# Kernel tuning notes

Hardware: AMD Instinct MI355X
Metric: run time of the kernel (lower is better)

The kernel has to match this reference:

```python
import jax, jax.numpy as jnp
import numpy as np

# Each of the 16 differentiable binary logic ops op_k(a,b) is a polynomial
# c0 + ca*a + cb*b + cab*(a*b). Rows follow the standard difflogic op table
# (op 3 = 'a' pass-through, matching the residual init in the source).
_OP2POLY = np.array([
    [0, 0, 0, 0],    # 0: False
    [0, 0, 0, 1],    # 1: a AND b
    [0, 1, 0, -1],   # 2: a AND NOT b
    [0, 1, 0, 0],    # 3: a
    [0, 0, 1, -1],   # 4: NOT a AND b
    [0, 0, 1, 0],    # 5: b
    [0, 1, 1, -2],   # 6: XOR
    [0, 1, 1, -1],   # 7: OR
    [1, -1, -1, 1],  # 8: NOR
    [1, -1, -1, 2],  # 9: XNOR
    [1, 0, -1, 0],   # 10: NOT b
    [1, 0, -1, 1],   # 11: a OR NOT b
    [1, -1, 0, 0],   # 12: NOT a
    [1, -1, 0, 1],   # 13: NOT a OR b
    [1, 0, 0, -1],   # 14: NAND
    [1, 0, 0, 0],    # 15: True
], dtype=np.float32)

KERNEL_SIZE, STRIDE, PADDING, GROUPS, TREE_DEPTH, TAU = 3, 1, 1, 1, 4, 1.0


def setup_inputs() -> dict:
    key = jax.random.key(0)
    k0, k1, k2, k3, k4 = jax.random.split(key, 5)
    B, Cin, H, W = 16, 64, 64, 64
    OC, N = 128, 2 ** TREE_DEPTH
    x = jax.random.uniform(k0, (B, Cin, H, W), dtype=jnp.float32)
    weights = jax.random.normal(k1, (OC, N - 1, 16), dtype=jnp.float32)
    ci = jax.random.randint(k2, (OC, N), 0, Cin // GROUPS, dtype=jnp.int32)
    px = jax.random.randint(k3, (OC, N), 0, KERNEL_SIZE, dtype=jnp.int32)
    py = jax.random.randint(k4, (OC, N), 0, KERNEL_SIZE, dtype=jnp.int32)
    return {"x": x, "weights": weights, "input_channel_indices": ci,
            "input_pos_x_indices": px, "input_pos_y_indices": py}


def _forward(x, weights, ci, px, py):
    B, Cin, H, W = x.shape
    OC = weights.shape[0]
    N = 2 ** TREE_DEPTH
    # Training-mode weights with straight-through estimator:
    # value = one_hot(argmax), gradient flows through softmax.
    w_soft = jax.nn.softmax(weights / TAU, axis=-1).astype(x.dtype)
    w_hard = jax.nn.one_hot(jnp.argmax(weights, axis=-1), 16, dtype=x.dtype)
    w = w_soft + jax.lax.stop_gradient(w_hard - w_soft)
    # [OC, num_gates, 4] polynomial coefficients over (1, a, b, ab)
    coeffs = jnp.einsum('ogk,kc->ogc', w, jnp.asarray(_OP2POLY, x.dtype))

    xp = jnp.pad(x, ((0, 0), (0, 0), (PADDING, PADDING), (PADDING, PADDING)))
    oh = (H + 2 * PADDING - KERNEL_SIZE) // STRIDE + 1
    ow = (W + 2 * PADDING - KERNEL_SIZE) // STRIDE + 1

    icpg = Cin // GROUPS
    group_of_oc = jnp.arange(OC, dtype=jnp.int32) // (OC // GROUPS)
    chan = group_of_oc[:, None] * icpg + ci                       # [OC, N]
    rows = (jnp.arange(oh, dtype=jnp.int32) * STRIDE)[None, None, :] + py[:, :, None]  # [OC,N,oh]
    cols = (jnp.arange(ow, dtype=jnp.int32) * STRIDE)[None, None, :] + px[:, :, None]  # [OC,N,ow]
    # Irregular per-output gather: [B, OC, N, oh, ow]
    vals = xp[:, chan[:, :, None, None], rows[:, :, :, None], cols[:, :, None, :]]

    # Binary tree of logic gates, level by level (gates stored leaf-level first).
    gate_off = 0
    for _ in range(TREE_DEPTH):
        n = vals.shape[2] // 2
        a, b = vals[:, :, 0::2], vals[:, :, 1::2]
        cc = coeffs[:, gate_off:gate_off + n]                     # [OC, n, 4]
        c0, ca, cb, cab = (cc[None, :, :, i, None, None] for i in range(4))
        vals = c0 + ca * a + cb * b + cab * (a * b)
        gate_off += n
    y = vals[:, :, 0]                                             # [B, OC, oh, ow]

    # 2x2 OR-pool (soft OR = 1 - prod(1 - v)), floor division of spatial dims.
    ph, pw = oh // 2, ow // 2
    y = y[:, :, :ph * 2, :pw * 2].reshape(B, OC, ph, 2, pw, 2)
    return 1.0 - jnp.prod(1.0 - y, axis=(3, 5))


def reference(x, weights, input_channel_indices, input_pos_x_indices, input_pos_y_indices):
    return _forward(x, weights, input_channel_indices, input_pos_x_indices, input_pos_y_indices)
```

## Files before the change

kernel.cpp:

```cpp
#include <hip/hip_runtime.h>

#define BATCH 16
#define CIN   64
#define H_    64
#define W_    64
#define IMG   (H_ * W_)
#define OCH   128
#define NLEAF 16
#define NGATE 15
#define PH    32
#define PW    32

#define XS_F   0
#define LEAF_F 24576
#define OPS_F  26624
#define ZF     27136
#define SMEM_F 27520

__device__ __constant__ __align__(16) float OP2POLY[16][4] = {
    {0, 0, 0, 0}, {0, 0, 0, 1}, {0, 1, 0, -1}, {0, 1, 0, 0},
    {0, 0, 1, -1}, {0, 0, 1, 0}, {0, 1, 1, -2}, {0, 1, 1, -1},
    {1, -1, -1, 1}, {1, -1, -1, 2}, {1, 0, -1, 0}, {1, 0, -1, 1},
    {1, -1, 0, 0}, {1, -1, 0, 1}, {1, 0, 0, -1}, {1, 0, 0, 0}};

static __device__ __forceinline__ int rfl_i(int v) {
    return __builtin_amdgcn_readfirstlane(v);
}

__global__ __launch_bounds__(1024) void logic_tree_lds(
    const float* __restrict__ x,
    const float* __restrict__ weights,
    const int* __restrict__ ci,
    const int* __restrict__ px,
    const int* __restrict__ py,
    float* __restrict__ out)
{
    __shared__ float smem[SMEM_F];
    int* smem_i = (int*)smem;
    unsigned char* smem_b = (unsigned char*)smem;

    const int blk   = blockIdx.x;
    const int b     = blk >> 4;
    const int strip = blk & 15;
    const int r0    = strip << 2;
    const int tid   = threadIdx.x;

    const float4* xb4 = reinterpret_cast<const float4*>(x + (size_t)b * (CIN * IMG));
#pragma unroll
    for (int i = 0; i < 6; ++i) {
        int fidx = tid + i * 1024;
        int ch   = fidx / 96;
        int rem  = fidx - ch * 96;
        int row  = rem >> 4;
        int c4   = rem & 15;
        int gr   = r0 - 1 + row;
        float4 val = make_float4(0.f, 0.f, 0.f, 0.f);
        if ((unsigned)gr < (unsigned)H_)
            val = xb4[((ch << 6) | gr) * 16 + c4];
        *reinterpret_cast<float4*>(&smem[ch * 384 + row * 64 + c4 * 4]) = val;
    }

    if (tid < 384) smem[ZF + tid] = 0.0f;

    for (int t = tid; t < OCH * NGATE; t += 1024) {
        const float* wp = weights + t * 16;
        int best = 0;
        float bv = wp[0];
#pragma unroll
        for (int k = 1; k < 16; ++k) {
            float v = wp[k];
            if (v > bv) { bv = v; best = k; }
        }
        int oc = t / 15, g = t - oc * 15;
        smem_b[OPS_F * 4 + oc * 16 + g] = (unsigned char)best;
        if (g == 14) smem_b[OPS_F * 4 + oc * 16 + 15] = 0;
    }

    for (int t = tid; t < OCH * NLEAF; t += 1024)
        smem_i[LEAF_F + t] = (ci[t] << 4) | (py[t] << 2) | px[t];

    __syncthreads();

    const int wave = tid >> 6;
    const int lane = tid & 63;

#pragma unroll 1
    for (int q = 0; q < 8; ++q) {
        const int oc = wave * 8 + q;

        const uint4 opsv =
            *reinterpret_cast<const uint4*>(&smem[OPS_F + oc * 4]);
        const unsigned ou[4] = {
            (unsigned)rfl_i((int)opsv.x), (unsigned)rfl_i((int)opsv.y),
            (unsigned)rfl_i((int)opsv.z), (unsigned)rfl_i((int)opsv.w)};
        float C[NGATE * 4];
#pragma unroll
        for (int g = 0; g < NGATE; ++g) {
            int op = (ou[g >> 2] >> ((g & 3) * 8)) & 255;
            const float4 cf = reinterpret_cast<const float4*>(OP2POLY)[op];
            C[4 * g + 0] = cf.x;
            C[4 * g + 1] = cf.y;
            C[4 * g + 2] = cf.z;
            C[4 * g + 3] = cf.w;
        }

        int base[NLEAF];
#pragma unroll
        for (int n = 0; n < NLEAF; ++n) {
            int pk = rfl_i(smem_i[LEAF_F + oc * 16 + n]);
            int ch = pk >> 4;
            int dy = ((pk >> 2) & 3) - 1;
            int dx = (pk & 3) - 1;
            int c  = lane + dx;
            int ccl = min(max(c, 0), W_ - 1);
            int bin = ch * 384 + (1 + dy) * 64 + ccl;
            int bz  = ZF + (1 + dy) * 64 + lane;
            base[n] = ((unsigned)c < (unsigned)W_) ? bin : bz;
        }

        const size_t obase =
            (((size_t)b * OCH + oc) * PH + (r0 >> 1)) * PW + (lane >> 1);

        float pprev = 0.0f;
#pragma unroll
        for (int r = 0; r < 4; ++r) {
            float v[NLEAF];
#pragma unroll
            for (int n = 0; n < NLEAF; ++n)
                v[n] = smem[base[n] + r * 64];

            int go = 0;
#pragma unroll
            for (int lev = 8; lev >= 1; lev >>= 1) {
#pragma unroll
                for (int t = 0; t < lev; ++t) {
                    float a  = v[2 * t];
                    float bb = v[2 * t + 1];
                    v[t] = C[(go + t) * 4] + C[(go + t) * 4 + 1] * a +
                           C[(go + t) * 4 + 2] * bb +
                           C[(go + t) * 4 + 3] * (a * bb);
                }
                go += lev;
            }

            float qv = 1.0f - v[0];
            if (r & 1) {
                float p  = pprev * qv;
                float pp = p * __shfl_xor(p, 1, 64);
                if (!(lane & 1))
                    out[obase + (size_t)(r >> 1) * PW] = 1.0f - pp;
            } else {
                pprev = qv;
            }
        }
    }
}

extern "C" void kernel_launch(void* const* d_in, const int* in_sizes, int n_in,
                              void* d_out, int out_size, void* d_ws, size_t ws_size,
                              hipStream_t stream) {
    const float* x       = (const float*)d_in[0];
    const float* weights = (const float*)d_in[1];
    const int*   ci      = (const int*)d_in[2];
    const int*   px      = (const int*)d_in[3];
    const int*   py      = (const int*)d_in[4];
    float* out = (float*)d_out;
    (void)d_ws; (void)ws_size;

    logic_tree_lds<<<BATCH * 16, 1024, 0, stream>>>(x, weights, ci, px, py, out);
}
```

Baseline: 101.0 us.

## Split weight argmax and leaf descriptors into a prep kernel, use packed float2 tree evaluation

Moves the per-block argmax over gate weights and the leaf index packing into a small prep kernel that writes expanded polynomial coefficients and precomputed LDS offsets to workspace. Previously all 256 blocks redid this work. The main kernel now reads coefficients as scalar float4 loads from global memory and evaluates two rows at once with float2 vectors so packed FMA can be used. It also remaps block indices so each XCD handles two batch images. The cost is an extra kernel launch and global/scalar loads inside the loop instead of register-resident coefficients.

```diff
diff --git a/kernel.cpp b/kernel.cpp
--- a/kernel.cpp
+++ b/kernel.cpp
@@ -11,11 +11,14 @@
 #define PH    32
 #define PW    32
 
-#define XS_F   0
-#define LEAF_F 24576
-#define OPS_F  26624
-#define ZF     27136
-#define SMEM_F 27520
+#define C_STRIDE_F4 16
+#define DESC_OFF    8192
+#define WS_NEED_BYTES ((DESC_OFF + OCH * NLEAF) * 4)
+
+#define ZF     24576
+#define SMEM_F (ZF + 384)
+
+typedef float f2 __attribute__((ext_vector_type(2)));
 
 __device__ __constant__ __align__(16) float OP2POLY[16][4] = {
     {0, 0, 0, 0}, {0, 0, 0, 1}, {0, 1, 0, -1}, {0, 1, 0, 0},
@@ -23,27 +26,47 @@
     {1, -1, -1, 1}, {1, -1, -1, 2}, {1, 0, -1, 0}, {1, 0, -1, 1},
     {1, -1, 0, 0}, {1, -1, 0, 1}, {1, 0, 0, -1}, {1, 0, 0, 0}};
 
-static __device__ __forceinline__ int rfl_i(int v) {
-    return __builtin_amdgcn_readfirstlane(v);
-}
-
-__global__ __launch_bounds__(1024) void logic_tree_lds(
-    const float* __restrict__ x,
+__global__ __launch_bounds__(1024) void prep(
     const float* __restrict__ weights,
     const int* __restrict__ ci,
     const int* __restrict__ px,
     const int* __restrict__ py,
+    float* __restrict__ ws)
+{
+    int t = blockIdx.x * 1024 + threadIdx.x;
+    if (t < OCH * NGATE) {
+        const float* wp = weights + t * 16;
+        int best = 0;
+        float bv = wp[0];
+#pragma unroll
+        for (int k = 1; k < 16; ++k) {
+            float v = wp[k];
+            if (v > bv) { bv = v; best = k; }
+        }
+        int oc = t / 15, g = t - oc * 15;
+        reinterpret_cast<float4*>(ws)[oc * C_STRIDE_F4 + g] =
+            reinterpret_cast<const float4*>(OP2POLY)[best];
+    } else if (t < OCH * NGATE + OCH * NLEAF) {
+        int t2 = t - OCH * NGATE;
+        int ch = ci[t2], pyy = py[t2], pxx = px[t2];
+        ((int*)ws)[DESC_OFF + t2] = ((ch * 384 + pyy * 64) << 4) | (pyy << 2) | pxx;
+    }
+}
+
+__global__ __launch_bounds__(1024) void logic_tree_main(
+    const float* __restrict__ x,
+    const float* __restrict__ ws,
     float* __restrict__ out)
 {
     __shared__ float smem[SMEM_F];
-    int* smem_i = (int*)smem;
-    unsigned char* smem_b = (unsigned char*)smem;
 
-    const int blk   = blockIdx.x;
-    const int b     = blk >> 4;
-    const int strip = blk & 15;
-    const int r0    = strip << 2;
-    const int tid   = threadIdx.x;
+    const int blk = blockIdx.x;
+    const int xcd = blk & 7;
+    const int j   = blk >> 3;
+    const int b   = (xcd << 1) | (j >> 4);
+    const int strip = j & 15;
+    const int r0  = strip << 2;
+    const int tid = threadIdx.x;
 
     const float4* xb4 = reinterpret_cast<const float4*>(x + (size_t)b * (CIN * IMG));
 #pragma unroll
@@ -57,28 +80,9 @@
         float4 val = make_float4(0.f, 0.f, 0.f, 0.f);
         if ((unsigned)gr < (unsigned)H_)
             val = xb4[((ch << 6) | gr) * 16 + c4];
-        *reinterpret_cast<float4*>(&smem[ch * 384 + row * 64 + c4 * 4]) = val;
+        *reinterpret_cast<float4*>(&smem[fidx * 4]) = val;
     }
-
     if (tid < 384) smem[ZF + tid] = 0.0f;
-
-    for (int t = tid; t < OCH * NGATE; t += 1024) {
-        const float* wp = weights + t * 16;
-        int best = 0;
-        float bv = wp[0];
-#pragma unroll
-        for (int k = 1; k < 16; ++k) {
-            float v = wp[k];
-            if (v > bv) { bv = v; best = k; }
-        }
-        int oc = t / 15, g = t - oc * 15;
-        smem_b[OPS_F * 4 + oc * 16 + g] = (unsigned char)best;
-        if (g == 14) smem_b[OPS_F * 4 + oc * 16 + 15] = 0;
-    }
-
-    for (int t = tid; t < OCH * NLEAF; t += 1024)
-        smem_i[LEAF_F + t] = (ci[t] << 4) | (py[t] << 2) | px[t];
-
     __syncthreads();
 
     const int wave = tid >> 6;
@@ -86,72 +90,48 @@
 
 #pragma unroll 1
     for (int q = 0; q < 8; ++q) {
-        const int oc = wave * 8 + q;
-
-        const uint4 opsv =
-            *reinterpret_cast<const uint4*>(&smem[OPS_F + oc * 4]);
-        const unsigned ou[4] = {
-            (unsigned)rfl_i((int)opsv.x), (unsigned)rfl_i((int)opsv.y),
-            (unsigned)rfl_i((int)opsv.z), (unsigned)rfl_i((int)opsv.w)};
-        float C[NGATE * 4];
-#pragma unroll
-        for (int g = 0; g < NGATE; ++g) {
-            int op = (ou[g >> 2] >> ((g & 3) * 8)) & 255;
-            const float4 cf = reinterpret_cast<const float4*>(OP2POLY)[op];
-            C[4 * g + 0] = cf.x;
-            C[4 * g + 1] = cf.y;
-            C[4 * g + 2] = cf.z;
-            C[4 * g + 3] = cf.w;
-        }
+        const int oc = __builtin_amdgcn_readfirstlane(wave * 8 + q);
+        const float4* C4 = reinterpret_cast<const float4*>(ws) + oc * C_STRIDE_F4;
+        const int*    D  = ((const int*)ws) + DESC_OFF + oc * NLEAF;
 
         int base[NLEAF];
 #pragma unroll
         for (int n = 0; n < NLEAF; ++n) {
-            int pk = rfl_i(smem_i[LEAF_F + oc * 16 + n]);
-            int ch = pk >> 4;
-            int dy = ((pk >> 2) & 3) - 1;
-            int dx = (pk & 3) - 1;
-            int c  = lane + dx;
+            int d  = D[n];
+            int c  = lane + (d & 3) - 1;
             int ccl = min(max(c, 0), W_ - 1);
-            int bin = ch * 384 + (1 + dy) * 64 + ccl;
-            int bz  = ZF + (1 + dy) * 64 + lane;
-            base[n] = ((unsigned)c < (unsigned)W_) ? bin : bz;
+            int bin = (d >> 4) + ccl;
+            int bz  = ZF + ((d >> 2) & 3) * 64 + lane;
+            base[n] = (c == ccl) ? bin : bz;
         }
 
         const size_t obase =
-            (((size_t)b * OCH + oc) * PH + (r0 >> 1)) * PW + (lane >> 1);
+            (((size_t)b * OCH + oc) * PH + (strip << 1)) * PW + (lane >> 1);
 
-        float pprev = 0.0f;
 #pragma unroll
-        for (int r = 0; r < 4; ++r) {
-            float v[NLEAF];
+        for (int rp = 0; rp < 2; ++rp) {
+            f2 v[NLEAF];
 #pragma unroll
-            for (int n = 0; n < NLEAF; ++n)
-                v[n] = smem[base[n] + r * 64];
-
+            for (int n = 0; n < NLEAF; ++n) {
+                v[n].x = smem[base[n] + rp * 128];
+                v[n].y = smem[base[n] + rp * 128 + 64];
+            }
             int go = 0;
 #pragma unroll
             for (int lev = 8; lev >= 1; lev >>= 1) {
 #pragma unroll
                 for (int t = 0; t < lev; ++t) {
-                    float a  = v[2 * t];
-                    float bb = v[2 * t + 1];
-                    v[t] = C[(go + t) * 4] + C[(go + t) * 4 + 1] * a +
-                           C[(go + t) * 4 + 2] * bb +
-                           C[(go + t) * 4 + 3] * (a * bb);
+                    const float4 cc = C4[go + t];
+                    f2 a  = v[2 * t];
+                    f2 bb = v[2 * t + 1];
+                    v[t] = cc.x + cc.y * a + cc.z * bb + cc.w * (a * bb);
                 }
                 go += lev;
             }
-
-            float qv = 1.0f - v[0];
-            if (r & 1) {
-                float p  = pprev * qv;
-                float pp = p * __shfl_xor(p, 1, 64);
-                if (!(lane & 1))
-                    out[obase + (size_t)(r >> 1) * PW] = 1.0f - pp;
-            } else {
-                pprev = qv;
-            }
+            float p  = (1.0f - v[0].x) * (1.0f - v[0].y);
+            float pp = p * __shfl_xor(p, 1, 64);
+            if (!(lane & 1))
+                out[obase + (size_t)rp * PW] = 1.0f - pp;
         }
     }
 }
@@ -165,7 +145,8 @@
     const int*   px      = (const int*)d_in[3];
     const int*   py      = (const int*)d_in[4];
     float* out = (float*)d_out;
-    (void)d_ws; (void)ws_size;
+    float* ws  = (float*)d_ws;
 
-    logic_tree_lds<<<BATCH * 16, 1024, 0, stream>>>(x, weights, ci, px, py, out);
+    prep<<<4, 1024, 0, stream>>>(weights, ci, px, py, ws);
+    logic_tree_main<<<BATCH * 16, 1024, 0, stream>>>(x, ws, out);
 }
```

Measured after the change: 98.80 us. 2.1% less time.
